# Optimization experiments

Measured on AMD Instinct MI355X. Metric: run time of the kernel, lower is better.

## Reference

```python
import jax, jax.numpy as jnp
import numpy as np
from jax import lax

# Normalized separable resample filter [1,3,3,1] (upfirdn2d.setup_filter divides by sum)
_F1 = np.array([1.0, 3.0, 3.0, 1.0]); _F1 /= _F1.sum()
_F2D = np.outer(_F1, _F1)  # 4x4, sums to 1
_CLAMP = 256.0
_LRELU_GAIN = np.sqrt(2.0)  # def_gain of lrelu in bias_act


def _depthwise(x, f2d):
    C = x.shape[1]
    k = jnp.broadcast_to(f2d[None, None], (C, 1, f2d.shape[0], f2d.shape[1])).astype(x.dtype)
    return lax.conv_general_dilated(x, k, (1, 1), [(0, 0), (0, 0)],
                                    dimension_numbers=('NCHW', 'OIHW', 'NCHW'),
                                    feature_group_count=C)


def _upfirdn_up2(x, pad, gain):
    # zero-insert upsample by 2, pad, FIR filter with given gain (upfirdn2d reference)
    B, C, H, W = x.shape
    x = jnp.pad(x.reshape(B, C, H, 1, W, 1), ((0, 0), (0, 0), (0, 0), (0, 1), (0, 0), (0, 1)))
    x = x.reshape(B, C, 2 * H, 2 * W)
    py0, py1, px0, px1 = pad
    x = jnp.pad(x, ((0, 0), (0, 0), (py0, py1), (px0, px1)))
    return _depthwise(x, jnp.asarray(_F2D * gain, x.dtype))


def _conv(x, w, pad):
    return lax.conv_general_dilated(x, w, (1, 1), [(pad, pad), (pad, pad)],
                                    dimension_numbers=('NCHW', 'OIHW', 'NCHW'))


def _mod_conv(x, weight, styles, demodulate, up, padding):
    # modulated_conv2d: modulate input by styles, shared-weight conv, demod output.
    # Mathematically identical to the fused grouped-conv path.
    if demodulate:
        w = weight[None] * styles[:, None, :, None, None]           # [B,Cout,Cin,kh,kw]
        dcoefs = lax.rsqrt(jnp.sum(w * w, axis=(2, 3, 4)) + 1e-8)   # [B,Cout]
    x = x * styles[:, :, None, None]
    if up == 2:
        # conv2d_resample(up=2): upfirdn2d(up=2, pad=(padding+2, padding+1), gain=4)
        # then conv with flipped weight (flip_weight=False)
        x = _upfirdn_up2(x, (padding + 2, padding + 1, padding + 2, padding + 1), 4.0)
        x = _conv(x, weight[:, :, ::-1, ::-1], 0)
    else:
        x = _conv(x, weight, padding)
    if demodulate:
        x = x * dcoefs[:, :, None, None]
    return x


def _bias_lrelu_clamp(x, b):
    x = x + b[None, :, None, None]
    x = jnp.where(x >= 0, x, 0.2 * x) * _LRELU_GAIN
    return jnp.clip(x, -_CLAMP, _CLAMP)


def setup_inputs() -> dict:
    key = jax.random.key(0)
    ks = jax.random.split(key, 16)
    B, CIN, COUT, WD, RES, IMG_CH = 8, 512, 512, 512, 64, 3
    return {
        'x': jax.random.normal(ks[0], (B, CIN, RES // 2, RES // 2), jnp.float32),
        'img': jax.random.normal(ks[1], (B, IMG_CH, RES // 2, RES // 2), jnp.float32),
        'ws': jax.random.normal(ks[2], (B, 3, WD), jnp.float32),
        'affine0_w': jax.random.normal(ks[3], (CIN, WD), jnp.float32),
        'affine0_b': jnp.ones((CIN,), jnp.float32),
        'weight0': jax.random.normal(ks[4], (COUT, CIN, 3, 3), jnp.float32),
        'bias0': jnp.zeros((COUT,), jnp.float32),
        'noise_strength0': jax.random.normal(ks[5], (1,), jnp.float32),
        'noise_const0': jax.random.normal(ks[6], (RES, RES), jnp.float32),
        'affine1_w': jax.random.normal(ks[7], (COUT, WD), jnp.float32),
        'affine1_b': jnp.ones((COUT,), jnp.float32),
        'weight1': jax.random.normal(ks[8], (COUT, COUT, 3, 3), jnp.float32),
        'bias1': jnp.zeros((COUT,), jnp.float32),
        'noise_strength1': jax.random.normal(ks[9], (1,), jnp.float32),
        'noise_const1': jax.random.normal(ks[10], (RES, RES), jnp.float32),
        'affine_rgb_w': jax.random.normal(ks[11], (COUT, WD), jnp.float32),
        'affine_rgb_b': jnp.ones((COUT,), jnp.float32),
        'weight_rgb': jax.random.normal(ks[12], (IMG_CH, COUT, 1, 1), jnp.float32),
        'bias_rgb': jnp.zeros((IMG_CH,), jnp.float32),
    }


def reference(x, img, ws, affine0_w, affine0_b, weight0, bias0, noise_strength0, noise_const0,
              affine1_w, affine1_b, weight1, bias1, noise_strength1, noise_const1,
              affine_rgb_w, affine_rgb_b, weight_rgb, bias_rgb):
    sg = 1.0 / np.sqrt(ws.shape[-1])  # FullyConnectedLayer weight_gain
    # conv0: up=2, demodulated, const noise, lrelu+clamp
    s0 = ws[:, 0] @ affine0_w.T * sg + affine0_b
    x = _mod_conv(x, weight0, s0, True, 2, 1)
    x = x + noise_const0[None, None] * noise_strength0[0]
    x = _bias_lrelu_clamp(x, bias0)
    # conv1: up=1
    s1 = ws[:, 1] @ affine1_w.T * sg + affine1_b
    x = _mod_conv(x, weight1, s1, True, 1, 1)
    x = x + noise_const1[None, None] * noise_strength1[0]
    x = _bias_lrelu_clamp(x, bias1)
    # skip: upsample img (upsample2d: pad=(2,1), gain=4)
    img = _upfirdn_up2(img, (2, 1, 2, 1), 4.0)
    # torgb: 1x1 modulated conv, no demod, styles scaled by 1/sqrt(Cin)
    srgb = (ws[:, 2] @ affine_rgb_w.T * sg + affine_rgb_b) * (1.0 / np.sqrt(weight_rgb.shape[1]))
    y = _mod_conv(x, weight_rgb, srgb, False, 1, 0)
    y = jnp.clip(y + bias_rgb[None, :, None, None], -_CLAMP, _CLAMP)
    img = img + y
    return (x, img)
```

## Files before the change

### kernel.cpp

```cpp
#include <hip/hip_runtime.h>
#include <hip/hip_bf16.h>
#include <stdint.h>

#define DEV __device__ __forceinline__

typedef float f32x4 __attribute__((ext_vector_type(4)));
typedef short s16x8 __attribute__((ext_vector_type(8)));
typedef __bf16 bf16x8 __attribute__((ext_vector_type(8)));
typedef unsigned short u16;

DEV u16 f2bf(float f) {
  uint32_t u = __builtin_bit_cast(uint32_t, f);
  u += 0x7FFFu + ((u >> 16) & 1u);
  return (u16)(u >> 16);
}

DEV void gload16(const void* g, void* l) {
  __builtin_amdgcn_global_load_lds((__attribute__((address_space(1))) void*)(g),
                                   (__attribute__((address_space(3))) void*)(l),
                                   16, 0, 0);
}

DEV f32x4 mfma16(s16x8 a, s16x8 b, f32x4 c) {
  return __builtin_amdgcn_mfma_f32_16x16x32_bf16(
      __builtin_bit_cast(bf16x8, a), __builtin_bit_cast(bf16x8, b), c, 0, 0, 0);
}

#define OFF_S0    0ul
#define OFF_S1    16384ul
#define OFF_SRGB  32768ul
#define OFF_D0    49152ul
#define OFF_D1    65536ul
#define OFF_WSQ0  81920ul
#define OFF_WSQ1  1130496ul
#define OFF_ZERO  2179072ul
#define OFF_X0M   2179328ul
#define OFF_G     10567936ul
#define OFF_W1T   29442304ul
#define OFF_X1M   34160896ul

__global__ void styles_kernel(const float* __restrict__ wsv,
                              const float* __restrict__ a0w, const float* __restrict__ a0b,
                              const float* __restrict__ a1w, const float* __restrict__ a1b,
                              const float* __restrict__ argw, const float* __restrict__ argb,
                              float* __restrict__ s0, float* __restrict__ s1,
                              float* __restrict__ srgb) {
  const int idx = blockIdx.x * 4 + (threadIdx.x >> 6);
  const int lane = threadIdx.x & 63;
  const int l = idx >> 12, rem = idx & 4095, b = rem >> 9, o = rem & 511;
  const float* aw = (l == 0) ? a0w : ((l == 1) ? a1w : argw);
  const float* wrow = wsv + (b * 3 + l) * 512;
  const float* arow = aw + o * 512;
  float acc = 0.f;
#pragma unroll
  for (int k = 0; k < 8; ++k) acc += wrow[lane + 64 * k] * arow[lane + 64 * k];
#pragma unroll
  for (int off = 32; off; off >>= 1) acc += __shfl_xor(acc, off);
  if (lane == 0) {
    const float sg = 0.04419417382415922f;
    if (l == 0)      s0[b * 512 + o] = acc * sg + a0b[o];
    else if (l == 1) s1[b * 512 + o] = acc * sg + a1b[o];
    else             srgb[b * 512 + o] = (acc * sg + argb[o]) * sg;
  }
}

__global__ void prepG_kernel(const float* __restrict__ w0, u16* __restrict__ G,
                             float* __restrict__ wsq0) {
  const int idx = blockIdx.x * 256 + threadIdx.x;
  float w[9], sq = 0.f;
#pragma unroll
  for (int t = 0; t < 9; ++t) { w[t] = w0[idx * 9 + t]; sq += w[t] * w[t]; }
  wsq0[idx] = sq;
  const float kk[4] = {0.25f, 0.75f, 0.75f, 0.25f};
  float G2[6][6];
#pragma unroll
  for (int sy = 0; sy < 6; ++sy)
#pragma unroll
    for (int sx = 0; sx < 6; ++sx) {
      float a = 0.f;
#pragma unroll
      for (int uy = 0; uy < 3; ++uy) {
        const int ay = sy - uy;
        if (ay < 0 || ay > 3) continue;
#pragma unroll
        for (int ux = 0; ux < 3; ++ux) {
          const int ax = sx - ux;
          if (ax < 0 || ax > 3) continue;
          a += kk[ay] * kk[ax] * w[(2 - uy) * 3 + (2 - ux)];
        }
      }
      G2[sy][sx] = a;
    }
#pragma unroll
  for (int py = 0; py < 2; ++py)
#pragma unroll
    for (int px = 0; px < 2; ++px)
#pragma unroll
      for (int dyi = 0; dyi < 3; ++dyi)
#pragma unroll
        for (int dxi = 0; dxi < 3; ++dxi)
          G[(size_t)(((py * 2 + px) * 9) + dyi * 3 + dxi) * 262144 + idx] =
              f2bf(G2[2 * dyi + 1 - py][2 * dxi + 1 - px]);
}

__global__ void prepW1_kernel(const float* __restrict__ w1, u16* __restrict__ w1t,
                              float* __restrict__ wsq1) {
  const int idx = blockIdx.x * 256 + threadIdx.x;
  float w[9], sq = 0.f;
#pragma unroll
  for (int t = 0; t < 9; ++t) { w[t] = w1[idx * 9 + t]; sq += w[t] * w[t]; }
  wsq1[idx] = sq;
#pragma unroll
  for (int t = 0; t < 9; ++t) w1t[(size_t)t * 262144 + idx] = f2bf(w[t]);
}

__global__ void dcoef_kernel(const float* __restrict__ s0, const float* __restrict__ s1,
                             const float* __restrict__ wsq0, const float* __restrict__ wsq1,
                             float* __restrict__ d0, float* __restrict__ d1) {
  const int idx = blockIdx.x * 4 + (threadIdx.x >> 6);
  const int lane = threadIdx.x & 63;
  const int layer = idx >> 12, rem = idx & 4095, b = rem >> 9, o = rem & 511;
  const float* s = layer ? s1 : s0;
  const float* wsq = layer ? wsq1 : wsq0;
  float acc = 0.f;
#pragma unroll
  for (int k = 0; k < 8; ++k) {
    const int c = lane + 64 * k;
    const float sv = s[b * 512 + c];
    acc += sv * sv * wsq[o * 512 + c];
  }
#pragma unroll
  for (int off = 32; off; off >>= 1) acc += __shfl_xor(acc, off);
  if (lane == 0) (layer ? d1 : d0)[b * 512 + o] = 1.f / sqrtf(acc + 1e-8f);
}

__global__ void x0m_kernel(const float* __restrict__ x, const float* __restrict__ s0,
                           u16* __restrict__ out) {
  __shared__ u16 t[32 * 514];
  const int b = blockIdx.x >> 5, h = blockIdx.x & 31;
  const int tid = threadIdx.x;
  const int w = tid & 31, cs = tid >> 5;
  for (int c0 = 0; c0 < 512; c0 += 8) {
    const int c = c0 + cs;
    t[w * 514 + c] = f2bf(x[((b * 512 + c) * 32 + h) * 32 + w] * s0[b * 512 + c]);
  }
  __syncthreads();
  const int base = ((b * 32 + h) * 32) * 512;
  for (int i = 0; i < 64; ++i) {
    const int idx = i * 256 + tid;
    out[base + idx] = t[(idx >> 9) * 514 + (idx & 511)];
  }
}

template <int H, bool CONV0>
__global__ __launch_bounds__(256, 2) void conv_mfma_kernel(
    const u16* __restrict__ xin, const u16* __restrict__ wt,
    const float* __restrict__ dcoef, const float* __restrict__ bias,
    const float* __restrict__ noise, const float* __restrict__ nstr,
    const float* __restrict__ s_next, float* __restrict__ out_f32,
    u16* __restrict__ out_bf16, const char* __restrict__ zerobuf) {
  constexpr int W = H;
  constexpr int WC = W + 2;
  constexpr int ROWS = CONV0 ? 10 : 6;
  constexpr int BU_REAL = 4 * ROWS * WC;
  constexpr int NB_IT = (BU_REAL + 255) / 256;
  constexpr int BU_PAD = NB_IT * 256;
  constexpr int A_OFF = BU_PAD * 16;
  __shared__ __align__(16) char smem[(BU_PAD + 2304) * 16];

  const int tid = threadIdx.x;
  const int lane = tid & 63;
  const int wid = tid >> 6;
  const int l15 = lane & 15;
  const int l4 = lane >> 4;

  int bid = blockIdx.x;
  const int obIdx = bid & 7; bid >>= 3;
  int tile, phase, b;
  if (CONV0) { tile = bid & 3; phase = (bid >> 2) & 3; b = bid >> 4; }
  else       { tile = bid & 15; phase = 0; b = bid >> 4; }
  const int obase = obIdx * 64;
  const int row0 = CONV0 ? (tile * 8 - 1) : (tile * 4 - 1);

  int boff[NB_IT];
  bool bval[NB_IT];
#pragma unroll
  for (int i = 0; i < NB_IT; ++i) {
    const int u = i * 256 + tid;
    const int row = u / (4 * WC);
    const int rem = u - row * (4 * WC);
    const int k8 = rem / WC;
    const int col = rem - k8 * WC;
    const int ir = row0 + row;
    const int ic = col - 1;
    bval[i] = (row < ROWS) && (ir >= 0) && (ir < H) && (ic >= 0) && (ic < W);
    boff[i] = (((b * H + ir) * W + ic) * 512 + k8 * 8) * 2;
  }

  int prow[4], pcol[4], ub[4];
#pragma unroll
  for (int bc = 0; bc < 4; ++bc) {
    const int p = wid * 64 + bc * 16 + l15;
    prow[bc] = CONV0 ? (p >> 5) : (p >> 6);
    pcol[bc] = CONV0 ? (p & 31) : (p & 63);
    ub[bc] = ((prow[bc] * 4 + l4) * WC + pcol[bc]) * 16;
  }

  const u16* wtp = wt + (CONV0 ? (size_t)phase * 9 * 262144 : 0);

  f32x4 acc[4][4];
  const f32x4 fz = {0.f, 0.f, 0.f, 0.f};
#pragma unroll
  for (int i = 0; i < 4; ++i)
#pragma unroll
    for (int j = 0; j < 4; ++j) acc[i][j] = fz;

  for (int c0 = 0; c0 < 512; c0 += 32) {
#pragma unroll
    for (int i = 0; i < NB_IT; ++i) {
      const void* src = bval[i] ? (const void*)((const char*)xin + (boff[i] + c0 * 2))
                                : (const void*)zerobuf;
      gload16(src, smem + (i * 256 + wid * 64) * 16);
    }
#pragma unroll
    for (int t = 0; t < 9; ++t) {
      const void* src = (const void*)(wtp + ((size_t)(t * 512 + obase + lane) * 512 + c0 + wid * 8));
      gload16(src, smem + A_OFF + (t * 256 + wid * 64) * 16);
    }
    __syncthreads();
#pragma unroll
    for (int t = 0; t < 9; ++t) {
      const int dyi = t / 3, dxi = t % 3;
      s16x8 bfr[4], afr[4];
#pragma unroll
      for (int bc = 0; bc < 4; ++bc)
        bfr[bc] = *(const s16x8*)(smem + (ub[bc] + (dyi * 4 * WC + dxi) * 16));
#pragma unroll
      for (int f = 0; f < 4; ++f)
        afr[f] = *(const s16x8*)(smem + A_OFF + t * 4096 + (l4 * 64 + f * 16 + l15) * 16);
#pragma unroll
      for (int f = 0; f < 4; ++f)
#pragma unroll
        for (int bc = 0; bc < 4; ++bc)
          acc[f][bc] = mfma16(afr[f], bfr[bc], acc[f][bc]);
    }
    __syncthreads();
  }

  const float ns = nstr[0];
#pragma unroll
  for (int f = 0; f < 4; ++f) {
    const int o = obase + f * 16 + l4 * 4;
    const f32x4 dc = *(const f32x4*)(dcoef + b * 512 + o);
    const f32x4 bs = *(const f32x4*)(bias + o);
    f32x4 sn = fz;
    if constexpr (CONV0) sn = *(const f32x4*)(s_next + b * 512 + o);
#pragma unroll
    for (int bc = 0; bc < 4; ++bc) {
      int jy, jx;
      if constexpr (CONV0) {
        jy = 2 * (tile * 8 + prow[bc]) + (phase >> 1);
        jx = 2 * pcol[bc] + (phase & 1);
      } else {
        jy = tile * 4 + prow[bc];
        jx = pcol[bc];
      }
      const float nz = noise[jy * 64 + jx] * ns;
      float v[4];
#pragma unroll
      for (int r = 0; r < 4; ++r) {
        float xv = acc[f][bc][r] * dc[r] + nz + bs[r];
        xv = (xv < 0.f ? 0.2f * xv : xv) * 1.4142135623730951f;
        v[r] = fminf(fmaxf(xv, -256.f), 256.f);
      }
      if constexpr (CONV0) {
        ushort4 pk;
        pk.x = f2bf(v[0] * sn[0]);
        pk.y = f2bf(v[1] * sn[1]);
        pk.z = f2bf(v[2] * sn[2]);
        pk.w = f2bf(v[3] * sn[3]);
        *(ushort4*)(out_bf16 + ((size_t)((b * 64 + jy) * 64 + jx) * 512 + o)) = pk;
      } else {
#pragma unroll
        for (int r = 0; r < 4; ++r)
          out_f32[((size_t)(b * 512 + o + r) * 64 + jy) * 64 + jx] = v[r];
      }
    }
  }
}

__global__ void torgb_kernel(const float* __restrict__ xw, const float* __restrict__ img,
                             const float* __restrict__ srgb, const float* __restrict__ wrgb,
                             const float* __restrict__ brgb, float* __restrict__ imgout) {
  __shared__ float red[4][3][64];
  const int b = blockIdx.x >> 6, jy = blockIdx.x & 63;
  const int tid = threadIdx.x;
  const int jx = tid & 63, cg = tid >> 6;
  float p0 = 0.f, p1 = 0.f, p2 = 0.f;
  const float* xb = xw + ((size_t)(b * 512 + cg * 128) * 64 + jy) * 64 + jx;
  const float* sb = srgb + b * 512 + cg * 128;
  for (int i = 0; i < 128; ++i) {
    const float xs = xb[(size_t)i * 4096] * sb[i];
    const int c = cg * 128 + i;
    p0 += xs * wrgb[c];
    p1 += xs * wrgb[512 + c];
    p2 += xs * wrgb[1024 + c];
  }
  red[cg][0][jx] = p0; red[cg][1][jx] = p1; red[cg][2][jx] = p2;
  __syncthreads();
  if (cg == 0) {
    const int qy = jy >> 1, qx = jx >> 1;
    int ry[2]; float wy[2];
    if ((jy & 1) == 0) { ry[0] = qy - 1; wy[0] = 0.25f; ry[1] = qy; wy[1] = 0.75f; }
    else               { ry[0] = qy;     wy[0] = 0.75f; ry[1] = qy + 1; wy[1] = 0.25f; }
    int rx[2]; float wx[2];
    if ((jx & 1) == 0) { rx[0] = qx - 1; wx[0] = 0.25f; rx[1] = qx; wx[1] = 0.75f; }
    else               { rx[0] = qx;     wx[0] = 0.75f; rx[1] = qx + 1; wx[1] = 0.25f; }
#pragma unroll
    for (int o = 0; o < 3; ++o) {
      float y = red[0][o][jx] + red[1][o][jx] + red[2][o][jx] + red[3][o][jx] + brgb[o];
      y = fminf(fmaxf(y, -256.f), 256.f);
      float iv = 0.f;
#pragma unroll
      for (int a = 0; a < 2; ++a)
#pragma unroll
        for (int e = 0; e < 2; ++e)
          if (ry[a] >= 0 && ry[a] < 32 && rx[e] >= 0 && rx[e] < 32)
            iv += wy[a] * wx[e] * img[((b * 3 + o) * 32 + ry[a]) * 32 + rx[e]];
      imgout[((b * 3 + o) * 64 + jy) * 64 + jx] = y + iv;
    }
  }
}

extern "C" void kernel_launch(void* const* d_in, const int* in_sizes, int n_in,
                              void* d_out, int out_size, void* d_ws, size_t ws_size,
                              hipStream_t stream) {
  (void)in_sizes; (void)n_in; (void)out_size; (void)ws_size;
  const float* x    = (const float*)d_in[0];
  const float* img  = (const float*)d_in[1];
  const float* wsv  = (const float*)d_in[2];
  const float* a0w  = (const float*)d_in[3];
  const float* a0b  = (const float*)d_in[4];
  const float* w0   = (const float*)d_in[5];
  const float* b0   = (const float*)d_in[6];
  const float* ns0  = (const float*)d_in[7];
  const float* nc0  = (const float*)d_in[8];
  const float* a1w  = (const float*)d_in[9];
  const float* a1b  = (const float*)d_in[10];
  const float* w1   = (const float*)d_in[11];
  const float* b1   = (const float*)d_in[12];
  const float* ns1  = (const float*)d_in[13];
  const float* nc1  = (const float*)d_in[14];
  const float* argw = (const float*)d_in[15];
  const float* argb = (const float*)d_in[16];
  const float* wrgb = (const float*)d_in[17];
  const float* brgb = (const float*)d_in[18];

  char* wsb = (char*)d_ws;
  float* s0   = (float*)(wsb + OFF_S0);
  float* s1   = (float*)(wsb + OFF_S1);
  float* srgb = (float*)(wsb + OFF_SRGB);
  float* dd0  = (float*)(wsb + OFF_D0);
  float* dd1  = (float*)(wsb + OFF_D1);
  float* wsq0 = (float*)(wsb + OFF_WSQ0);
  float* wsq1 = (float*)(wsb + OFF_WSQ1);
  char*  zero = wsb + OFF_ZERO;
  u16*   x0m  = (u16*)(wsb + OFF_X0M);
  u16*   G    = (u16*)(wsb + OFF_G);
  u16*   w1t  = (u16*)(wsb + OFF_W1T);
  u16*   x1m  = (u16*)(wsb + OFF_X1M);

  float* out_x   = (float*)d_out;
  float* out_img = out_x + 16777216;

  hipMemsetAsync(zero, 0, 256, stream);
  styles_kernel<<<3072, 256, 0, stream>>>(wsv, a0w, a0b, a1w, a1b, argw, argb, s0, s1, srgb);
  prepG_kernel<<<1024, 256, 0, stream>>>(w0, G, wsq0);
  prepW1_kernel<<<1024, 256, 0, stream>>>(w1, w1t, wsq1);
  dcoef_kernel<<<2048, 256, 0, stream>>>(s0, s1, wsq0, wsq1, dd0, dd1);
  x0m_kernel<<<256, 256, 0, stream>>>(x, s0, x0m);
  conv_mfma_kernel<32, true><<<1024, 256, 0, stream>>>(
      x0m, G, dd0, b0, nc0, ns0, s1, nullptr, x1m, zero);
  conv_mfma_kernel<64, false><<<1024, 256, 0, stream>>>(
      x1m, w1t, dd1, b1, nc1, ns1, nullptr, out_x, nullptr, zero);
  torgb_kernel<<<512, 256, 0, stream>>>(out_x, img, srgb, wrgb, brgb, out_img);
}
```

Baseline: 442.5 us.

## Software-pipeline conv MFMA loop with double-buffered LDS and uniform 8x32 tiles

Restructures the conv main loop so that weight slices (per tap) and activation tiles (per channel chunk) are double-buffered in LDS. The next loads are issued while MFMAs run on the current buffer, with fine-grained vmcnt waits and barriers per tap. The conv1 tiling changes from 4x64 to 8x32 so that both convs share one 10x34 halo layout, which lowers halo overhead for conv1. The cost is a barrier pair per tap, plus s_setprio hints and a fully unrolled phase schedule that raises code size and register pressure.

Measured after the change: 431.1 us. 2.6% less time.

```diff
diff --git a/kernel.cpp b/kernel.cpp
--- a/kernel.cpp
+++ b/kernel.cpp
@@ -160,13 +160,7 @@
     const float* __restrict__ s_next, float* __restrict__ out_f32,
     u16* __restrict__ out_bf16, const char* __restrict__ zerobuf) {
   constexpr int W = H;
-  constexpr int WC = W + 2;
-  constexpr int ROWS = CONV0 ? 10 : 6;
-  constexpr int BU_REAL = 4 * ROWS * WC;
-  constexpr int NB_IT = (BU_REAL + 255) / 256;
-  constexpr int BU_PAD = NB_IT * 256;
-  constexpr int A_OFF = BU_PAD * 16;
-  __shared__ __align__(16) char smem[(BU_PAD + 2304) * 16];
+  __shared__ __align__(16) char smem[57344];
 
   const int tid = threadIdx.x;
   const int lane = tid & 63;
@@ -176,37 +170,44 @@
 
   int bid = blockIdx.x;
   const int obIdx = bid & 7; bid >>= 3;
-  int tile, phase, b;
-  if (CONV0) { tile = bid & 3; phase = (bid >> 2) & 3; b = bid >> 4; }
-  else       { tile = bid & 15; phase = 0; b = bid >> 4; }
+  int tile, phase, b, rt, ct;
+  if (CONV0) { tile = bid & 3; phase = (bid >> 2) & 3; b = bid >> 4; rt = tile; ct = 0; }
+  else       { tile = bid & 15; phase = 0; b = bid >> 4; rt = tile >> 1; ct = tile & 1; }
   const int obase = obIdx * 64;
-  const int row0 = CONV0 ? (tile * 8 - 1) : (tile * 4 - 1);
-
-  int boff[NB_IT];
-  bool bval[NB_IT];
-#pragma unroll
-  for (int i = 0; i < NB_IT; ++i) {
+  const int row0 = rt * 8 - 1;
+  const int col0 = ct * 32 - 1;
+
+  size_t boff[6];
+  bool bvalid[6];
+#pragma unroll
+  for (int i = 0; i < 6; ++i) {
     const int u = i * 256 + tid;
-    const int row = u / (4 * WC);
-    const int rem = u - row * (4 * WC);
-    const int k8 = rem / WC;
-    const int col = rem - k8 * WC;
+    const int row = u / 136;
+    const int rem = u - row * 136;
+    const int k8 = rem / 34;
+    const int col = rem - k8 * 34;
     const int ir = row0 + row;
-    const int ic = col - 1;
-    bval[i] = (row < ROWS) && (ir >= 0) && (ir < H) && (ic >= 0) && (ic < W);
-    boff[i] = (((b * H + ir) * W + ic) * 512 + k8 * 8) * 2;
-  }
-
-  int prow[4], pcol[4], ub[4];
+    const int ic = col0 + col;
+    bvalid[i] = (u < 1360) && (ir >= 0) && (ir < H) && (ic >= 0) && (ic < W);
+    boff[i] = ((size_t)((b * H + ir) * W + ic) * 512 + k8 * 8) * 2;
+  }
+
+  int ub[4], jy[4], jx[4];
 #pragma unroll
   for (int bc = 0; bc < 4; ++bc) {
     const int p = wid * 64 + bc * 16 + l15;
-    prow[bc] = CONV0 ? (p >> 5) : (p >> 6);
-    pcol[bc] = CONV0 ? (p & 31) : (p & 63);
-    ub[bc] = ((prow[bc] * 4 + l4) * WC + pcol[bc]) * 16;
+    const int pr = p >> 5, pc = p & 31;
+    ub[bc] = ((pr * 4 + l4) * 34 + pc) * 16;
+    if (CONV0) { jy[bc] = 2 * (rt * 8 + pr) + (phase >> 1); jx[bc] = 2 * pc + (phase & 1); }
+    else       { jy[bc] = rt * 8 + pr; jx[bc] = ct * 32 + pc; }
   }
 
   const u16* wtp = wt + (CONV0 ? (size_t)phase * 9 * 262144 : 0);
+  const char* wtA = (const char*)wtp;
+  const char* xin_c = (const char*)xin;
+  const size_t aoff = ((size_t)(obase + lane) * 512 + (size_t)wid * 8) * 2;
+  const int ldsAw = wid * 1024;
+  const int ldsBw = wid * 1024;
 
   f32x4 acc[4][4];
   const f32x4 fz = {0.f, 0.f, 0.f, 0.f};
@@ -215,37 +216,74 @@
 #pragma unroll
     for (int j = 0; j < 4; ++j) acc[i][j] = fz;
 
-  for (int c0 = 0; c0 < 512; c0 += 32) {
-#pragma unroll
-    for (int i = 0; i < NB_IT; ++i) {
-      const void* src = bval[i] ? (const void*)((const char*)xin + (boff[i] + c0 * 2))
-                                : (const void*)zerobuf;
-      gload16(src, smem + (i * 256 + wid * 64) * 16);
-    }
-#pragma unroll
-    for (int t = 0; t < 9; ++t) {
-      const void* src = (const void*)(wtp + ((size_t)(t * 512 + obase + lane) * 512 + c0 + wid * 8));
-      gload16(src, smem + A_OFF + (t * 256 + wid * 64) * 16);
-    }
-    __syncthreads();
-#pragma unroll
-    for (int t = 0; t < 9; ++t) {
-      const int dyi = t / 3, dxi = t % 3;
-      s16x8 bfr[4], afr[4];
-#pragma unroll
-      for (int bc = 0; bc < 4; ++bc)
-        bfr[bc] = *(const s16x8*)(smem + (ub[bc] + (dyi * 4 * WC + dxi) * 16));
-#pragma unroll
-      for (int f = 0; f < 4; ++f)
-        afr[f] = *(const s16x8*)(smem + A_OFF + t * 4096 + (l4 * 64 + f * 16 + l15) * 16);
-#pragma unroll
-      for (int f = 0; f < 4; ++f)
-#pragma unroll
-        for (int bc = 0; bc < 4; ++bc)
-          acc[f][bc] = mfma16(afr[f], bfr[bc], acc[f][bc]);
-    }
-    __syncthreads();
-  }
+  gload16(wtA + aoff, smem + ldsAw);
+#pragma unroll
+  for (int ch = 0; ch < 6; ++ch) {
+    const void* src = bvalid[ch] ? (const void*)(xin_c + boff[ch]) : (const void*)zerobuf;
+    gload16(src, smem + 8192 + ch * 4096 + ldsBw);
+  }
+  asm volatile("s_waitcnt vmcnt(0)" ::: "memory");
+  __builtin_amdgcn_s_barrier();
+
+#define CONV_PH(tt, NW, DO_A, DO_B, AIC)                                        \
+  {                                                                             \
+    if (DO_A) {                                                                 \
+      const int nt_ = ((tt) == 8) ? 0 : ((tt) + 1);                             \
+      const int nc_ = ((tt) == 8) ? ((AIC) + 1) : (AIC);                        \
+      const int nap_ = ((AIC) + (tt) + 1) & 1;                                  \
+      gload16(wtA + aoff + (size_t)nt_ * 524288 + (size_t)nc_ * 64,             \
+              smem + nap_ * 4096 + ldsAw);                                      \
+    }                                                                           \
+    if (DO_B && (tt) < 6) {                                                     \
+      const void* src_ = bvalid[(tt)] ? (const void*)(xin_c + boff[(tt)] +      \
+                            (size_t)((AIC) + 1) * 64) : (const void*)zerobuf;   \
+      gload16(src_, smem + 8192 + (((AIC) + 1) & 1) * 24576 +                   \
+              (tt) * 4096 + ldsBw);                                             \
+    }                                                                           \
+    asm volatile("s_waitcnt vmcnt(" NW ")" ::: "memory");                       \
+    __builtin_amdgcn_s_barrier();                                               \
+    const char* Ab_ = smem + (((AIC) + (tt)) & 1) * 4096;                       \
+    const char* Bb_ = smem + 8192 + ((AIC) & 1) * 24576;                        \
+    s16x8 afr_[4], bfr_[4];                                                     \
+    _Pragma("unroll")                                                           \
+    for (int f_ = 0; f_ < 4; ++f_)                                              \
+      afr_[f_] = *(const s16x8*)(Ab_ + (l4 * 64 + f_ * 16 + l15) * 16);         \
+    _Pragma("unroll")                                                           \
+    for (int bc_ = 0; bc_ < 4; ++bc_)                                           \
+      bfr_[bc_] = *(const s16x8*)(Bb_ + ub[bc_] +                               \
+                                  (((tt) / 3) * 136 + ((tt) % 3)) * 16);        \
+    __builtin_amdgcn_s_setprio(1);                                              \
+    _Pragma("unroll")                                                           \
+    for (int f_ = 0; f_ < 4; ++f_)                                              \
+      _Pragma("unroll")                                                         \
+      for (int bc_ = 0; bc_ < 4; ++bc_)                                         \
+        acc[f_][bc_] = mfma16(afr_[f_], bfr_[bc_], acc[f_][bc_]);               \
+    __builtin_amdgcn_s_setprio(0);                                              \
+    __builtin_amdgcn_s_barrier();                                               \
+  }
+
+#pragma unroll 1
+  for (int c0i = 0; c0i < 15; ++c0i) {
+    CONV_PH(0, "2", true, true, c0i)
+    CONV_PH(1, "3", true, true, c0i)
+    CONV_PH(2, "3", true, true, c0i)
+    CONV_PH(3, "3", true, true, c0i)
+    CONV_PH(4, "3", true, true, c0i)
+    CONV_PH(5, "3", true, true, c0i)
+    CONV_PH(6, "2", true, true, c0i)
+    CONV_PH(7, "1", true, true, c0i)
+    CONV_PH(8, "1", true, true, c0i)
+  }
+  CONV_PH(0, "1", true, false, 15)
+  CONV_PH(1, "1", true, false, 15)
+  CONV_PH(2, "1", true, false, 15)
+  CONV_PH(3, "1", true, false, 15)
+  CONV_PH(4, "1", true, false, 15)
+  CONV_PH(5, "1", true, false, 15)
+  CONV_PH(6, "1", true, false, 15)
+  CONV_PH(7, "1", true, false, 15)
+  CONV_PH(8, "0", false, false, 15)
+#undef CONV_PH
 
   const float ns = nstr[0];
 #pragma unroll
@@ -257,15 +295,7 @@
     if constexpr (CONV0) sn = *(const f32x4*)(s_next + b * 512 + o);
 #pragma unroll
     for (int bc = 0; bc < 4; ++bc) {
-      int jy, jx;
-      if constexpr (CONV0) {
-        jy = 2 * (tile * 8 + prow[bc]) + (phase >> 1);
-        jx = 2 * pcol[bc] + (phase & 1);
-      } else {
-        jy = tile * 4 + prow[bc];
-        jx = pcol[bc];
-      }
-      const float nz = noise[jy * 64 + jx] * ns;
+      const float nz = noise[jy[bc] * 64 + jx[bc]] * ns;
       float v[4];
 #pragma unroll
       for (int r = 0; r < 4; ++r) {
@@ -279,11 +309,11 @@
         pk.y = f2bf(v[1] * sn[1]);
         pk.z = f2bf(v[2] * sn[2]);
         pk.w = f2bf(v[3] * sn[3]);
-        *(ushort4*)(out_bf16 + ((size_t)((b * 64 + jy) * 64 + jx) * 512 + o)) = pk;
+        *(ushort4*)(out_bf16 + ((size_t)((b * 64 + jy[bc]) * 64 + jx[bc]) * 512 + o)) = pk;
       } else {
 #pragma unroll
         for (int r = 0; r < 4; ++r)
-          out_f32[((size_t)(b * 512 + o + r) * 64 + jy) * 64 + jx] = v[r];
+          out_f32[((size_t)(b * 512 + o + r) * 64 + jy[bc]) * 64 + jx[bc]] = v[r];
       }
     }
   }
```

## Split upsample conv into phase-decomposed transposed conv plus separate FIR pass

Applied to the files above, without the earlier changes.

Conv0 previously folded the 4x4 FIR into a 6x6 composite kernel, giving four output phases with nine taps each (36 MFMA taps per output group). It now computes the transposed 3x3 conv through polyphase decomposition with 4+2+2+1 = 9 taps on a 33x33 grid, writes a bf16 intermediate, and a new FIR kernel applies the 4x4 blur together with demod, noise, bias, lrelu, clamp and next-layer style scaling. This cuts the matmul FLOPs for conv0 by about four times. In exchange it adds a large intermediate round-trip through memory, an extra launch, and an extra bf16 rounding of the pre-FIR values.

Result: slower. 473.3 us (+7.0%).

```diff
diff --git a/kernel.cpp b/kernel.cpp
--- a/kernel.cpp
+++ b/kernel.cpp
@@ -7,6 +7,7 @@
 typedef float f32x4 __attribute__((ext_vector_type(4)));
 typedef short s16x8 __attribute__((ext_vector_type(8)));
 typedef __bf16 bf16x8 __attribute__((ext_vector_type(8)));
+typedef unsigned short us8 __attribute__((ext_vector_type(8)));
 typedef unsigned short u16;
 
 DEV u16 f2bf(float f) {
@@ -14,6 +15,7 @@
   u += 0x7FFFu + ((u >> 16) & 1u);
   return (u16)(u >> 16);
 }
+DEV float bf2f(u16 h) { return __builtin_bit_cast(float, (uint32_t)h << 16); }
 
 DEV void gload16(const void* g, void* l) {
   __builtin_amdgcn_global_load_lds((__attribute__((address_space(1))) void*)(g),
@@ -35,9 +37,10 @@
 #define OFF_WSQ1  1130496ul
 #define OFF_ZERO  2179072ul
 #define OFF_X0M   2179328ul
-#define OFF_G     10567936ul
-#define OFF_W1T   29442304ul
-#define OFF_X1M   34160896ul
+#define OFF_W0T   10567936ul
+#define OFF_W1T   15286528ul
+#define OFF_ZZ    20005120ul
+#define OFF_X1M   55689472ul
 
 __global__ void styles_kernel(const float* __restrict__ wsv,
                               const float* __restrict__ a0w, const float* __restrict__ a0b,
@@ -64,54 +67,15 @@
   }
 }
 
-__global__ void prepG_kernel(const float* __restrict__ w0, u16* __restrict__ G,
-                             float* __restrict__ wsq0) {
+__global__ void prepWT_kernel(const float* __restrict__ w, u16* __restrict__ wt,
+                              float* __restrict__ wsq) {
   const int idx = blockIdx.x * 256 + threadIdx.x;
-  float w[9], sq = 0.f;
-#pragma unroll
-  for (int t = 0; t < 9; ++t) { w[t] = w0[idx * 9 + t]; sq += w[t] * w[t]; }
-  wsq0[idx] = sq;
-  const float kk[4] = {0.25f, 0.75f, 0.75f, 0.25f};
-  float G2[6][6];
-#pragma unroll
-  for (int sy = 0; sy < 6; ++sy)
-#pragma unroll
-    for (int sx = 0; sx < 6; ++sx) {
-      float a = 0.f;
-#pragma unroll
-      for (int uy = 0; uy < 3; ++uy) {
-        const int ay = sy - uy;
-        if (ay < 0 || ay > 3) continue;
-#pragma unroll
-        for (int ux = 0; ux < 3; ++ux) {
-          const int ax = sx - ux;
-          if (ax < 0 || ax > 3) continue;
-          a += kk[ay] * kk[ax] * w[(2 - uy) * 3 + (2 - ux)];
-        }
-      }
-      G2[sy][sx] = a;
-    }
-#pragma unroll
-  for (int py = 0; py < 2; ++py)
-#pragma unroll
-    for (int px = 0; px < 2; ++px)
-#pragma unroll
-      for (int dyi = 0; dyi < 3; ++dyi)
-#pragma unroll
-        for (int dxi = 0; dxi < 3; ++dxi)
-          G[(size_t)(((py * 2 + px) * 9) + dyi * 3 + dxi) * 262144 + idx] =
-              f2bf(G2[2 * dyi + 1 - py][2 * dxi + 1 - px]);
-}
-
-__global__ void prepW1_kernel(const float* __restrict__ w1, u16* __restrict__ w1t,
-                              float* __restrict__ wsq1) {
-  const int idx = blockIdx.x * 256 + threadIdx.x;
-  float w[9], sq = 0.f;
-#pragma unroll
-  for (int t = 0; t < 9; ++t) { w[t] = w1[idx * 9 + t]; sq += w[t] * w[t]; }
-  wsq1[idx] = sq;
-#pragma unroll
-  for (int t = 0; t < 9; ++t) w1t[(size_t)t * 262144 + idx] = f2bf(w[t]);
+  float v[9], sq = 0.f;
+#pragma unroll
+  for (int t = 0; t < 9; ++t) { v[t] = w[idx * 9 + t]; sq += v[t] * v[t]; }
+  wsq[idx] = sq;
+#pragma unroll
+  for (int t = 0; t < 9; ++t) wt[(size_t)t * 262144 + idx] = f2bf(v[t]);
 }
 
 __global__ void dcoef_kernel(const float* __restrict__ s0, const float* __restrict__ s1,
@@ -152,61 +116,230 @@
   }
 }
 
-template <int H, bool CONV0>
-__global__ __launch_bounds__(256, 2) void conv_mfma_kernel(
+template <int PH>
+DEV void phaseconv_body(char* smem, int tid, int lane, int wid, int l15, int l4,
+                        int obase, int tile, int b,
+                        const char* xin_c, const char* wt_c, u16* __restrict__ zz,
+                        const char* __restrict__ zerobuf) {
+  constexpr int NT = (PH == 0) ? 4 : ((PH == 3) ? 1 : 2);
+  constexpr int SLt[4][4] = {{8, 6, 2, 0}, {7, 1, 0, 0}, {5, 3, 0, 0}, {4, 0, 0, 0}};
+  constexpr int TYt[4][4] = {{0, 0, 1, 1}, {0, 1, 0, 0}, {1, 1, 0, 0}, {1, 0, 0, 0}};
+  constexpr int TXt[4][4] = {{0, 1, 0, 1}, {1, 1, 0, 0}, {0, 1, 0, 0}, {1, 0, 0, 0}};
+  constexpr int A_OFF = 24576;
+
+  const int p0 = tile * 256;
+  const int r0 = (p0 * 993) >> 15;
+  const int row0 = r0 - 1;
+
+  size_t boff[6];
+  bool bval[6];
+#pragma unroll
+  for (int i = 0; i < 6; ++i) {
+    const int u = i * 256 + tid;
+    const int row = u / 136;
+    const int rem = u - row * 136;
+    const int k8 = rem / 34;
+    const int col = rem - k8 * 34;
+    const int ir = row0 + row;
+    const int ic = col - 1;
+    bval[i] = (u < 1360) && (ir >= 0) && (ir < 32) && (ic >= 0) && (ic < 32);
+    boff[i] = ((size_t)((b * 32 + ir) * 32 + ic) * 512 + k8 * 8) * 2;
+  }
+
+  int ub[4], pp[4];
+#pragma unroll
+  for (int bc = 0; bc < 4; ++bc) {
+    const int p = p0 + wid * 64 + bc * 16 + l15;
+    pp[bc] = p;
+    const int qy = (p * 993) >> 15;
+    const int qx = p - qy * 33;
+    ub[bc] = (((qy - r0) * 4 + l4) * 34 + qx) * 16;
+  }
+
+  const size_t aoffb = ((size_t)(obase + lane) * 512 + (size_t)wid * 8) * 2;
+
+  f32x4 acc[4][4];
+  const f32x4 fz = {0.f, 0.f, 0.f, 0.f};
+#pragma unroll
+  for (int i = 0; i < 4; ++i)
+#pragma unroll
+    for (int j = 0; j < 4; ++j) acc[i][j] = fz;
+
+  for (int c0 = 0; c0 < 512; c0 += 32) {
+#pragma unroll
+    for (int i = 0; i < 6; ++i) {
+      const void* src = bval[i] ? (const void*)(xin_c + boff[i] + (size_t)c0 * 2)
+                                : (const void*)zerobuf;
+      gload16(src, smem + i * 4096 + wid * 1024);
+    }
+#pragma unroll
+    for (int t = 0; t < NT; ++t)
+      gload16(wt_c + (size_t)SLt[PH][t] * 524288 + aoffb + (size_t)c0 * 2,
+              smem + A_OFF + t * 4096 + wid * 1024);
+    __syncthreads();
+#pragma unroll
+    for (int t = 0; t < NT; ++t) {
+      s16x8 bfr[4], afr[4];
+#pragma unroll
+      for (int bc = 0; bc < 4; ++bc)
+        bfr[bc] = *(const s16x8*)(smem + ub[bc] + (TYt[PH][t] * 136 + TXt[PH][t]) * 16);
+#pragma unroll
+      for (int f = 0; f < 4; ++f)
+        afr[f] = *(const s16x8*)(smem + A_OFF + t * 4096 + (l4 * 64 + f * 16 + l15) * 16);
+#pragma unroll
+      for (int f = 0; f < 4; ++f)
+#pragma unroll
+        for (int bc = 0; bc < 4; ++bc)
+          acc[f][bc] = mfma16(afr[f], bfr[bc], acc[f][bc]);
+    }
+    __syncthreads();
+  }
+
+#pragma unroll
+  for (int f = 0; f < 4; ++f) {
+    const int o = obase + f * 16 + l4 * 4;
+#pragma unroll
+    for (int bc = 0; bc < 4; ++bc) {
+      if (pp[bc] < 1089) {
+        ushort4 pk;
+        pk.x = f2bf(acc[f][bc][0]);
+        pk.y = f2bf(acc[f][bc][1]);
+        pk.z = f2bf(acc[f][bc][2]);
+        pk.w = f2bf(acc[f][bc][3]);
+        *(ushort4*)(zz + ((size_t)(PH * 8 + b) * 1089 + pp[bc]) * 512 + o) = pk;
+      }
+    }
+  }
+}
+
+__global__ __launch_bounds__(256, 3) void phaseconv_kernel(
+    const u16* __restrict__ xin, const u16* __restrict__ wt, u16* __restrict__ zz,
+    const char* __restrict__ zerobuf) {
+  __shared__ __align__(16) char smem[40960];
+  const int tid = threadIdx.x;
+  const int lane = tid & 63, wid = tid >> 6, l15 = lane & 15, l4 = lane >> 4;
+  const int bid = blockIdx.x;
+  const int ph = bid / 320;
+  const int rr = bid - ph * 320;
+  const int obIdx = rr & 7;
+  const int r = rr >> 3;
+  const int tile = r % 5;
+  const int b = r / 5;
+  const int obase = obIdx * 64;
+  const char* xin_c = (const char*)xin;
+  const char* wt_c = (const char*)wt;
+  switch (ph) {
+    case 0: phaseconv_body<0>(smem, tid, lane, wid, l15, l4, obase, tile, b, xin_c, wt_c, zz, zerobuf); break;
+    case 1: phaseconv_body<1>(smem, tid, lane, wid, l15, l4, obase, tile, b, xin_c, wt_c, zz, zerobuf); break;
+    case 2: phaseconv_body<2>(smem, tid, lane, wid, l15, l4, obase, tile, b, xin_c, wt_c, zz, zerobuf); break;
+    default: phaseconv_body<3>(smem, tid, lane, wid, l15, l4, obase, tile, b, xin_c, wt_c, zz, zerobuf); break;
+  }
+}
+
+__global__ __launch_bounds__(256) void fir_kernel(
+    const u16* __restrict__ zz, const float* __restrict__ dc0,
+    const float* __restrict__ bias0, const float* __restrict__ noise0,
+    const float* __restrict__ ns0, const float* __restrict__ s1,
+    u16* __restrict__ x1m) {
+  const int u = blockIdx.x & 63, b = blockIdx.x >> 6;
+  const int tid = threadIdx.x;
+  const int v = tid & 63, cg0 = tid >> 6;
+  const float nz = noise0[u * 64 + v] * ns0[0];
+  const float kk[4] = {0.25f, 0.75f, 0.75f, 0.25f};
+
+  float wy[4], wx[4];
+  int ry[4], qy[4], rx[4], qx[4];
+#pragma unroll
+  for (int k = 0; k < 4; ++k) {
+    const int my = u - 1 + k;
+    wy[k] = (my >= 0) ? kk[k] : 0.f;
+    ry[k] = my & 1;
+    qy[k] = (my >= 0) ? (my >> 1) : 0;
+    const int mx = v - 1 + k;
+    wx[k] = (mx >= 0) ? kk[k] : 0.f;
+    rx[k] = mx & 1;
+    qx[k] = (mx >= 0) ? (mx >> 1) : 0;
+  }
+  size_t off16[16];
+  float w16[16];
+#pragma unroll
+  for (int ky = 0; ky < 4; ++ky)
+#pragma unroll
+    for (int kx = 0; kx < 4; ++kx) {
+      const int phn = ry[ky] * 2 + rx[kx];
+      off16[ky * 4 + kx] = ((size_t)(phn * 8 + b) * 1089 + qy[ky] * 33 + qx[kx]) * 512;
+      w16[ky * 4 + kx] = wy[ky] * wx[kx];
+    }
+
+  for (int cgi = 0; cgi < 16; ++cgi) {
+    const int c = cg0 * 8 + cgi * 32;
+    float a[8] = {0.f, 0.f, 0.f, 0.f, 0.f, 0.f, 0.f, 0.f};
+#pragma unroll
+    for (int t = 0; t < 16; ++t) {
+      const us8 zv = *(const us8*)(zz + off16[t] + c);
+      const float w = w16[t];
+#pragma unroll
+      for (int r = 0; r < 8; ++r) a[r] = fmaf(w, bf2f(zv[r]), a[r]);
+    }
+    const float* dcp = dc0 + b * 512 + c;
+    const float* bp = bias0 + c;
+    const float* sp = s1 + b * 512 + c;
+    us8 pk;
+#pragma unroll
+    for (int r = 0; r < 8; ++r) {
+      float xv = a[r] * dcp[r] + nz + bp[r];
+      xv = (xv < 0.f ? 0.2f * xv : xv) * 1.4142135623730951f;
+      xv = fminf(fmaxf(xv, -256.f), 256.f);
+      pk[r] = f2bf(xv * sp[r]);
+    }
+    *(us8*)(x1m + ((size_t)((b * 64 + u) * 64 + v) * 512 + c)) = pk;
+  }
+}
+
+__global__ __launch_bounds__(256, 2) void conv1_kernel(
     const u16* __restrict__ xin, const u16* __restrict__ wt,
     const float* __restrict__ dcoef, const float* __restrict__ bias,
     const float* __restrict__ noise, const float* __restrict__ nstr,
-    const float* __restrict__ s_next, float* __restrict__ out_f32,
-    u16* __restrict__ out_bf16, const char* __restrict__ zerobuf) {
-  constexpr int W = H;
-  constexpr int WC = W + 2;
-  constexpr int ROWS = CONV0 ? 10 : 6;
-  constexpr int BU_REAL = 4 * ROWS * WC;
-  constexpr int NB_IT = (BU_REAL + 255) / 256;
-  constexpr int BU_PAD = NB_IT * 256;
-  constexpr int A_OFF = BU_PAD * 16;
-  __shared__ __align__(16) char smem[(BU_PAD + 2304) * 16];
-
+    float* __restrict__ out_f32, const char* __restrict__ zerobuf) {
+  __shared__ __align__(16) char smem[65536];
   const int tid = threadIdx.x;
-  const int lane = tid & 63;
-  const int wid = tid >> 6;
-  const int l15 = lane & 15;
-  const int l4 = lane >> 4;
+  const int lane = tid & 63, wid = tid >> 6, l15 = lane & 15, l4 = lane >> 4;
 
   int bid = blockIdx.x;
   const int obIdx = bid & 7; bid >>= 3;
-  int tile, phase, b;
-  if (CONV0) { tile = bid & 3; phase = (bid >> 2) & 3; b = bid >> 4; }
-  else       { tile = bid & 15; phase = 0; b = bid >> 4; }
+  const int tile = bid & 15;
+  const int b = bid >> 4;
   const int obase = obIdx * 64;
-  const int row0 = CONV0 ? (tile * 8 - 1) : (tile * 4 - 1);
-
-  int boff[NB_IT];
-  bool bval[NB_IT];
-#pragma unroll
-  for (int i = 0; i < NB_IT; ++i) {
+  const int row0 = tile * 4 - 1;
+
+  size_t boff[7];
+  bool bval[7];
+#pragma unroll
+  for (int i = 0; i < 7; ++i) {
     const int u = i * 256 + tid;
-    const int row = u / (4 * WC);
-    const int rem = u - row * (4 * WC);
-    const int k8 = rem / WC;
-    const int col = rem - k8 * WC;
+    const int row = u / 264;
+    const int rem = u - row * 264;
+    const int k8 = rem / 66;
+    const int col = rem - k8 * 66;
     const int ir = row0 + row;
     const int ic = col - 1;
-    bval[i] = (row < ROWS) && (ir >= 0) && (ir < H) && (ic >= 0) && (ic < W);
-    boff[i] = (((b * H + ir) * W + ic) * 512 + k8 * 8) * 2;
-  }
-
-  int prow[4], pcol[4], ub[4];
+    bval[i] = (row < 6) && (ir >= 0) && (ir < 64) && (ic >= 0) && (ic < 64);
+    boff[i] = ((size_t)((b * 64 + ir) * 64 + ic) * 512 + k8 * 8) * 2;
+  }
+
+  int ub[4], jy[4], jx[4];
 #pragma unroll
   for (int bc = 0; bc < 4; ++bc) {
     const int p = wid * 64 + bc * 16 + l15;
-    prow[bc] = CONV0 ? (p >> 5) : (p >> 6);
-    pcol[bc] = CONV0 ? (p & 31) : (p & 63);
-    ub[bc] = ((prow[bc] * 4 + l4) * WC + pcol[bc]) * 16;
-  }
-
-  const u16* wtp = wt + (CONV0 ? (size_t)phase * 9 * 262144 : 0);
+    const int pr = p >> 6, pc = p & 63;
+    ub[bc] = ((pr * 4 + l4) * 66 + pc) * 16;
+    jy[bc] = tile * 4 + pr;
+    jx[bc] = pc;
+  }
+
+  const char* wt_c = (const char*)wt;
+  const char* xin_c = (const char*)xin;
+  const size_t aoffb = ((size_t)(obase + lane) * 512 + (size_t)wid * 8) * 2;
 
   f32x4 acc[4][4];
   const f32x4 fz = {0.f, 0.f, 0.f, 0.f};
@@ -217,16 +350,15 @@
 
   for (int c0 = 0; c0 < 512; c0 += 32) {
 #pragma unroll
-    for (int i = 0; i < NB_IT; ++i) {
-      const void* src = bval[i] ? (const void*)((const char*)xin + (boff[i] + c0 * 2))
+    for (int i = 0; i < 7; ++i) {
+      const void* src = bval[i] ? (const void*)(xin_c + boff[i] + (size_t)c0 * 2)
                                 : (const void*)zerobuf;
-      gload16(src, smem + (i * 256 + wid * 64) * 16);
-    }
-#pragma unroll
-    for (int t = 0; t < 9; ++t) {
-      const void* src = (const void*)(wtp + ((size_t)(t * 512 + obase + lane) * 512 + c0 + wid * 8));
-      gload16(src, smem + A_OFF + (t * 256 + wid * 64) * 16);
-    }
+      gload16(src, smem + i * 4096 + wid * 1024);
+    }
+#pragma unroll
+    for (int t = 0; t < 9; ++t)
+      gload16(wt_c + (size_t)t * 524288 + aoffb + (size_t)c0 * 2,
+              smem + 28672 + t * 4096 + wid * 1024);
     __syncthreads();
 #pragma unroll
     for (int t = 0; t < 9; ++t) {
@@ -234,10 +366,10 @@
       s16x8 bfr[4], afr[4];
 #pragma unroll
       for (int bc = 0; bc < 4; ++bc)
-        bfr[bc] = *(const s16x8*)(smem + (ub[bc] + (dyi * 4 * WC + dxi) * 16));
+        bfr[bc] = *(const s16x8*)(smem + ub[bc] + (dyi * 264 + dxi) * 16);
 #pragma unroll
       for (int f = 0; f < 4; ++f)
-        afr[f] = *(const s16x8*)(smem + A_OFF + t * 4096 + (l4 * 64 + f * 16 + l15) * 16);
+        afr[f] = *(const s16x8*)(smem + 28672 + t * 4096 + (l4 * 64 + f * 16 + l15) * 16);
 #pragma unroll
       for (int f = 0; f < 4; ++f)
 #pragma unroll
@@ -253,37 +385,15 @@
     const int o = obase + f * 16 + l4 * 4;
     const f32x4 dc = *(const f32x4*)(dcoef + b * 512 + o);
     const f32x4 bs = *(const f32x4*)(bias + o);
-    f32x4 sn = fz;
-    if constexpr (CONV0) sn = *(const f32x4*)(s_next + b * 512 + o);
 #pragma unroll
     for (int bc = 0; bc < 4; ++bc) {
-      int jy, jx;
-      if constexpr (CONV0) {
-        jy = 2 * (tile * 8 + prow[bc]) + (phase >> 1);
-        jx = 2 * pcol[bc] + (phase & 1);
-      } else {
-        jy = tile * 4 + prow[bc];
-        jx = pcol[bc];
-      }
-      const float nz = noise[jy * 64 + jx] * ns;
-      float v[4];
+      const float nz = noise[jy[bc] * 64 + jx[bc]] * ns;
 #pragma unroll
       for (int r = 0; r < 4; ++r) {
         float xv = acc[f][bc][r] * dc[r] + nz + bs[r];
         xv = (xv < 0.f ? 0.2f * xv : xv) * 1.4142135623730951f;
-        v[r] = fminf(fmaxf(xv, -256.f), 256.f);
-      }
-      if constexpr (CONV0) {
-        ushort4 pk;
-        pk.x = f2bf(v[0] * sn[0]);
-        pk.y = f2bf(v[1] * sn[1]);
-        pk.z = f2bf(v[2] * sn[2]);
-        pk.w = f2bf(v[3] * sn[3]);
-        *(ushort4*)(out_bf16 + ((size_t)((b * 64 + jy) * 64 + jx) * 512 + o)) = pk;
-      } else {
-#pragma unroll
-        for (int r = 0; r < 4; ++r)
-          out_f32[((size_t)(b * 512 + o + r) * 64 + jy) * 64 + jx] = v[r];
+        xv = fminf(fmaxf(xv, -256.f), 256.f);
+        out_f32[((size_t)(b * 512 + o + r) * 64 + jy[bc]) * 64 + jx[bc]] = xv;
       }
     }
   }
@@ -366,8 +476,9 @@
   float* wsq1 = (float*)(wsb + OFF_WSQ1);
   char*  zero = wsb + OFF_ZERO;
   u16*   x0m  = (u16*)(wsb + OFF_X0M);
-  u16*   G    = (u16*)(wsb + OFF_G);
+  u16*   w0t  = (u16*)(wsb + OFF_W0T);
   u16*   w1t  = (u16*)(wsb + OFF_W1T);
+  u16*   zz   = (u16*)(wsb + OFF_ZZ);
   u16*   x1m  = (u16*)(wsb + OFF_X1M);
 
   float* out_x   = (float*)d_out;
@@ -375,13 +486,12 @@
 
   hipMemsetAsync(zero, 0, 256, stream);
   styles_kernel<<<3072, 256, 0, stream>>>(wsv, a0w, a0b, a1w, a1b, argw, argb, s0, s1, srgb);
-  prepG_kernel<<<1024, 256, 0, stream>>>(w0, G, wsq0);
-  prepW1_kernel<<<1024, 256, 0, stream>>>(w1, w1t, wsq1);
+  prepWT_kernel<<<1024, 256, 0, stream>>>(w0, w0t, wsq0);
+  prepWT_kernel<<<1024, 256, 0, stream>>>(w1, w1t, wsq1);
   dcoef_kernel<<<2048, 256, 0, stream>>>(s0, s1, wsq0, wsq1, dd0, dd1);
   x0m_kernel<<<256, 256, 0, stream>>>(x, s0, x0m);
-  conv_mfma_kernel<32, true><<<1024, 256, 0, stream>>>(
-      x0m, G, dd0, b0, nc0, ns0, s1, nullptr, x1m, zero);
-  conv_mfma_kernel<64, false><<<1024, 256, 0, stream>>>(
-      x1m, w1t, dd1, b1, nc1, ns1, nullptr, out_x, nullptr, zero);
+  phaseconv_kernel<<<1280, 256, 0, stream>>>(x0m, w0t, zz, zero);
+  fir_kernel<<<512, 256, 0, stream>>>(zz, dd0, b0, nc0, ns0, s1, x1m);
+  conv1_kernel<<<1024, 256, 0, stream>>>(x1m, w1t, dd1, b1, nc1, ns1, out_x, zero);
   torgb_kernel<<<512, 256, 0, stream>>>(out_x, img, srgb, wrgb, brgb, out_img);
 }
```
